# Optimization experiments

Measured on AMD Instinct MI355X. Metric: run time of the kernel, lower is better.

The kernel has to match this reference:

```python
import jax, jax.numpy as jnp
import numpy as np
from jax import lax

EPS = 0.1
CHANNEL = 1


def _sobel_kernels(channel):
    # sobel: 3x3, each row [-0.5, 0, 0.5] -> varies along width (w)
    s = jnp.array([[-0.5, 0.0, 0.5],
                   [-0.5, 0.0, 0.5],
                   [-0.5, 0.0, 0.5]], dtype=jnp.float32)
    kx = jnp.broadcast_to(s, (3, 3, 3))          # [d,h,w], constant over d,h; torch sobel.repeat(c,1,3,1,1)
    ky = jnp.broadcast_to(s.T, (3, 3, 3))        # varies along h
    kz = jnp.stack([jnp.full((3, 3), -0.5, jnp.float32),
                    jnp.zeros((3, 3), jnp.float32),
                    jnp.full((3, 3), 0.5, jnp.float32)], axis=0)  # varies along d
    def rep(k):
        return jnp.tile(k[None, None], (channel, 1, 1, 1, 1))  # [C,1,3,3,3] OIDHW
    return rep(kx), rep(ky), rep(kz)


def _grad3(x_pad, kernel, channel):
    # x_pad: [N,C,D+2,H+2,W+2]; cross-correlation matching F.conv3d, padding=0
    return lax.conv_general_dilated(
        x_pad, kernel, window_strides=(1, 1, 1), padding='VALID',
        dimension_numbers=('NCDHW', 'OIDHW', 'NCDHW'),
        feature_group_count=channel)


def setup_inputs() -> dict:
    key = jax.random.key(0)
    k1, k2 = jax.random.split(key)
    shape = (1, 1, 192, 224, 192)
    I = jax.random.normal(k1, shape, dtype=jnp.float32)
    J = jax.random.normal(k2, shape, dtype=jnp.float32)
    return {"I": I, "J": J}


def reference(I, J):
    kx, ky, kz = _sobel_kernels(CHANNEL)
    pad = ((0, 0), (0, 0), (1, 1), (1, 1), (1, 1))
    I_pad = jnp.pad(I, pad, mode='edge')  # ReplicationPad3d(1)
    J_pad = jnp.pad(J, pad, mode='edge')
    Ix = _grad3(I_pad, kx, CHANNEL)
    Iy = _grad3(I_pad, ky, CHANNEL)
    Iz = _grad3(I_pad, kz, CHANNEL)
    Jx = _grad3(J_pad, kx, CHANNEL)
    Jy = _grad3(J_pad, ky, CHANNEL)
    Jz = _grad3(J_pad, kz, CHANNEL)
    I_mag = Ix * Ix + Iy * Iy + Iz * Iz + EPS * EPS
    J_mag = Jx * Jx + Jy * Jy + Jz * Jz + EPS * EPS
    dot = Ix * Jx + Iy * Jy + Iz * Jz  # == sum over concat channel dim (C=1)
    ngf = (dot * dot) / (I_mag * J_mag)
    return jnp.mean(1.0 - ngf)
```

## Files before the change

### kernel.cpp

```cpp
#include <hip/hip_runtime.h>
#include <stdint.h>

#define DD 192
#define HH 224
#define WW 192
#define PLANE (HH*WW)
#define TOTAL (DD*HH*WW)

#define DSEG 6
#define NSEG (DD/DSEG)
#define NT 64
#define HPAIRS (HH/2)
#define NBLOCKS (HPAIRS*NSEG)

#define TILEF (4*WW)
#define BUFF (2*TILEF)
#define NPIECE 384
#define GUARD 4

typedef __attribute__((address_space(3))) uint32_t lds_t;
typedef __attribute__((address_space(1))) const uint32_t glb_t;

#define WAITV6()  asm volatile("s_waitcnt vmcnt(6)" ::: "memory")
#define WAITV0()  asm volatile("s_waitcnt vmcnt(0)" ::: "memory")
#define LGKM0()   asm volatile("s_waitcnt lgkmcnt(0)" ::: "memory")

struct PP {
    float IPT[6], IPS[6], IHD[6];
    float JPT[6], JPS[6], JHD[6];
};

__global__ __launch_bounds__(NT) void ngf_main_kernel(
    const float* __restrict__ I, const float* __restrict__ J,
    float* __restrict__ partial)
{
    __shared__ __align__(16) float lds[GUARD + 2 * BUFF + 4];
    const float EPS2 = 0.04f;

    int lane = threadIdx.x;

    int bid0 = blockIdx.x;
    int bid  = (bid0 & 7) * (NBLOCKS / 8) + (bid0 >> 3);

    int hb   = 2 * (bid % HPAIRS);
    int seg  = bid / HPAIRS;
    int ds   = seg * DSEG;

    const float* sp[6];
    int lo[6];
    #pragma unroll
    for (int m = 0; m < 6; ++m) {
        int p = lane + m * NT;
        int inp = (p >= NPIECE / 2) ? 1 : 0;
        int q   = p - inp * (NPIECE / 2);
        int r   = q / 48, c = q % 48;
        int srow = min(max(hb - 1 + r, 0), HH - 1);
        sp[m] = (inp ? J : I) + srow * WW + c * 4;
        lo[m] = GUARD + 4 * p;
    }

    auto stage = [&](int dp, int buf) {
        size_t poff = (size_t)dp * PLANE;
        #pragma unroll
        for (int m = 0; m < 6; ++m) {
            __builtin_amdgcn_global_load_lds((glb_t*)(sp[m] + poff),
                (lds_t*)(&lds[buf * BUFF + lo[m]]), 16, 0, 0);
        }
    };

    int l3 = 3 * lane;
    bool b0  = (lane == 0);
    bool b63 = (lane == 63);

    auto combine = [&](int buf) -> PP {
        PP P;
        #pragma unroll
        for (int j = 0; j < 6; ++j) {
            P.IPT[j] = 0.f; P.IPS[j] = 0.f; P.IHD[j] = 0.f;
            P.JPT[j] = 0.f; P.JPS[j] = 0.f; P.JHD[j] = 0.f;
        }
        const float* base = &lds[GUARD + buf * BUFF];
        #pragma unroll
        for (int b = 0; b < 4; ++b) {
            const float* BI = base + b * WW;
            const float* BJ = BI + TILEF;
            {
                float Lr = BI[l3 - 1];
                float x0 = BI[l3], x1 = BI[l3 + 1], x2 = BI[l3 + 2];
                float Rr = BI[l3 + 3];
                float L = b0  ? x0 : Lr;
                float R = b63 ? x2 : Rr;
                float s0 = L  + x0 + x1;
                float s1 = x0 + x1 + x2;
                float s2 = x1 + x2 + R;
                float t0 = x1 - L;
                float t1 = x2 - x0;
                float t2 = R  - x1;
                if (b <= 2) {
                    P.IPT[0] += t0; P.IPT[1] += t1; P.IPT[2] += t2;
                    P.IPS[0] += s0; P.IPS[1] += s1; P.IPS[2] += s2;
                    if (b == 0) { P.IHD[0] -= s0; P.IHD[1] -= s1; P.IHD[2] -= s2; }
                    if (b == 2) { P.IHD[0] += s0; P.IHD[1] += s1; P.IHD[2] += s2; }
                }
                if (b >= 1) {
                    P.IPT[3] += t0; P.IPT[4] += t1; P.IPT[5] += t2;
                    P.IPS[3] += s0; P.IPS[4] += s1; P.IPS[5] += s2;
                    if (b == 1) { P.IHD[3] -= s0; P.IHD[4] -= s1; P.IHD[5] -= s2; }
                    if (b == 3) { P.IHD[3] += s0; P.IHD[4] += s1; P.IHD[5] += s2; }
                }
            }
            {
                float Lr = BJ[l3 - 1];
                float x0 = BJ[l3], x1 = BJ[l3 + 1], x2 = BJ[l3 + 2];
                float Rr = BJ[l3 + 3];
                float L = b0  ? x0 : Lr;
                float R = b63 ? x2 : Rr;
                float s0 = L  + x0 + x1;
                float s1 = x0 + x1 + x2;
                float s2 = x1 + x2 + R;
                float t0 = x1 - L;
                float t1 = x2 - x0;
                float t2 = R  - x1;
                if (b <= 2) {
                    P.JPT[0] += t0; P.JPT[1] += t1; P.JPT[2] += t2;
                    P.JPS[0] += s0; P.JPS[1] += s1; P.JPS[2] += s2;
                    if (b == 0) { P.JHD[0] -= s0; P.JHD[1] -= s1; P.JHD[2] -= s2; }
                    if (b == 2) { P.JHD[0] += s0; P.JHD[1] += s1; P.JHD[2] += s2; }
                }
                if (b >= 1) {
                    P.JPT[3] += t0; P.JPT[4] += t1; P.JPT[5] += t2;
                    P.JPS[3] += s0; P.JPS[4] += s1; P.JPS[5] += s2;
                    if (b == 1) { P.JHD[3] -= s0; P.JHD[4] -= s1; P.JHD[5] -= s2; }
                    if (b == 3) { P.JHD[3] += s0; P.JHD[4] += s1; P.JHD[5] += s2; }
                }
            }
        }
        return P;
    };

    auto dcl = [&](int m) { return min(max(ds + m, 0), DD - 1); };

    float acc = 0.0f;
    PP p[3];

    auto ngf = [&](int k) {
        int sa = k % 3, sb2 = (k + 1) % 3, sc = (k + 2) % 3;
        #pragma unroll
        for (int j = 0; j < 6; ++j) {
            float Ix = p[sa].IPT[j] + p[sb2].IPT[j] + p[sc].IPT[j];
            float Iy = p[sa].IHD[j] + p[sb2].IHD[j] + p[sc].IHD[j];
            float Iz = p[sc].IPS[j] - p[sa].IPS[j];
            float Jx = p[sa].JPT[j] + p[sb2].JPT[j] + p[sc].JPT[j];
            float Jy = p[sa].JHD[j] + p[sb2].JHD[j] + p[sc].JHD[j];
            float Jz = p[sc].JPS[j] - p[sa].JPS[j];
            float Imag = fmaf(Ix, Ix, fmaf(Iy, Iy, fmaf(Iz, Iz, EPS2)));
            float Jmag = fmaf(Jx, Jx, fmaf(Jy, Jy, fmaf(Jz, Jz, EPS2)));
            float dot  = fmaf(Ix, Jx, fmaf(Iy, Jy, Iz * Jz));
            acc += 1.0f - (dot * dot) * __builtin_amdgcn_rcpf(Imag * Jmag);
        }
    };

    stage(dcl(-1), 0);
    stage(dcl(0), 1);
    WAITV6();
    p[0] = combine(0);
    LGKM0();
    stage(dcl(1), 0);
    WAITV6();
    p[1] = combine(1);
    LGKM0();
    stage(dcl(2), 1);

    #pragma unroll
    for (int k = 0; k < DSEG; ++k) {
        int buf = k & 1;
        if (k < DSEG - 1) { WAITV6(); }
        else             { WAITV0(); }
        __builtin_amdgcn_s_setprio(1);
        p[(k + 2) % 3] = combine(buf);
        __builtin_amdgcn_s_setprio(0);
        if (k <= DSEG - 3) {
            LGKM0();
            stage(dcl(k + 3), buf);
        }
        __builtin_amdgcn_s_setprio(1);
        ngf(k);
        __builtin_amdgcn_s_setprio(0);
    }

    #pragma unroll
    for (int o = 32; o > 0; o >>= 1)
        acc += __shfl_down(acc, o, 64);
    if (lane == 0)
        partial[bid] = acc;
}

__global__ __launch_bounds__(256) void ngf_reduce_kernel(
    const float* __restrict__ partial, float* __restrict__ out)
{
    double acc = 0.0;
    for (int i = threadIdx.x; i < NBLOCKS; i += blockDim.x)
        acc += (double)partial[i];

    #pragma unroll
    for (int o = 32; o > 0; o >>= 1)
        acc += __shfl_down(acc, o, 64);

    __shared__ double smem[4];
    int lane = threadIdx.x & 63;
    int wid  = threadIdx.x >> 6;
    if (lane == 0) smem[wid] = acc;
    __syncthreads();
    if (threadIdx.x == 0) {
        double s = smem[0] + smem[1] + smem[2] + smem[3];
        out[0] = (float)(s / (double)TOTAL);
    }
}

extern "C" void kernel_launch(void* const* d_in, const int* in_sizes, int n_in,
                              void* d_out, int out_size, void* d_ws, size_t ws_size,
                              hipStream_t stream)
{
    const float* I = (const float*)d_in[0];
    const float* J = (const float*)d_in[1];
    float* out = (float*)d_out;
    float* partial = (float*)d_ws;

    ngf_main_kernel<<<NBLOCKS, NT, 0, stream>>>(I, J, partial);
    ngf_reduce_kernel<<<1, 256, 0, stream>>>(partial, out);
}
```

Measured before the change: 29.18 us.

## Replace LDS double-buffered async staging with direct global loads

Removes the global_load_lds staging of four-row tiles into double-buffered shared memory, along with the manual waitcnt and setprio scheduling. Each lane now reads its three voxels plus neighbours straight from global memory through the cache, with edge clamping folded into precomputed offsets. This drops the LDS round trip and the explicit sync. The cost is that prefetch overlap is left to the compiler and hardware, and the loads become strided scalar loads per lane rather than 16-byte vector transfers.

Result: slower. 49.57 us (+69.8%).

```diff
diff --git a/kernel.cpp b/kernel.cpp
--- a/kernel.cpp
+++ b/kernel.cpp
@@ -13,17 +13,6 @@
 #define HPAIRS (HH/2)
 #define NBLOCKS (HPAIRS*NSEG)
 
-#define TILEF (4*WW)
-#define BUFF (2*TILEF)
-#define NPIECE 384
-#define GUARD 4
-
-typedef __attribute__((address_space(3))) uint32_t lds_t;
-typedef __attribute__((address_space(1))) const uint32_t glb_t;
-
-#define WAITV6()  asm volatile("s_waitcnt vmcnt(6)" ::: "memory")
-#define WAITV0()  asm volatile("s_waitcnt vmcnt(0)" ::: "memory")
-#define LGKM0()   asm volatile("s_waitcnt lgkmcnt(0)" ::: "memory")
 
 struct PP {
     float IPT[6], IPS[6], IHD[6];
@@ -34,7 +23,6 @@
     const float* __restrict__ I, const float* __restrict__ J,
     float* __restrict__ partial)
 {
-    __shared__ __align__(16) float lds[GUARD + 2 * BUFF + 4];
     const float EPS2 = 0.04f;
 
     int lane = threadIdx.x;
@@ -46,50 +34,31 @@
     int seg  = bid / HPAIRS;
     int ds   = seg * DSEG;
 
-    const float* sp[6];
-    int lo[6];
+    int srow[4];
     #pragma unroll
-    for (int m = 0; m < 6; ++m) {
-        int p = lane + m * NT;
-        int inp = (p >= NPIECE / 2) ? 1 : 0;
-        int q   = p - inp * (NPIECE / 2);
-        int r   = q / 48, c = q % 48;
-        int srow = min(max(hb - 1 + r, 0), HH - 1);
-        sp[m] = (inp ? J : I) + srow * WW + c * 4;
-        lo[m] = GUARD + 4 * p;
-    }
+    for (int r = 0; r < 4; ++r)
+        srow[r] = min(max(hb - 1 + r, 0), HH - 1);
 
-    auto stage = [&](int dp, int buf) {
-        size_t poff = (size_t)dp * PLANE;
-        #pragma unroll
-        for (int m = 0; m < 6; ++m) {
-            __builtin_amdgcn_global_load_lds((glb_t*)(sp[m] + poff),
-                (lds_t*)(&lds[buf * BUFF + lo[m]]), 16, 0, 0);
-        }
-    };
+    int l3   = 3 * lane;
+    int offL = l3 + ((lane == 0)  ? 0 : -1);
+    int offR = l3 + ((lane == 63) ? 2 :  3);
 
-    int l3 = 3 * lane;
-    bool b0  = (lane == 0);
-    bool b63 = (lane == 63);
-
-    auto combine = [&](int buf) -> PP {
+    auto combine = [&](int dp) -> PP {
         PP P;
         #pragma unroll
         for (int j = 0; j < 6; ++j) {
             P.IPT[j] = 0.f; P.IPS[j] = 0.f; P.IHD[j] = 0.f;
             P.JPT[j] = 0.f; P.JPS[j] = 0.f; P.JHD[j] = 0.f;
         }
-        const float* base = &lds[GUARD + buf * BUFF];
+        size_t poff = (size_t)dp * PLANE;
         #pragma unroll
         for (int b = 0; b < 4; ++b) {
-            const float* BI = base + b * WW;
-            const float* BJ = BI + TILEF;
+            const float* RI = I + poff + srow[b] * WW;
+            const float* RJ = J + poff + srow[b] * WW;
             {
-                float Lr = BI[l3 - 1];
-                float x0 = BI[l3], x1 = BI[l3 + 1], x2 = BI[l3 + 2];
-                float Rr = BI[l3 + 3];
-                float L = b0  ? x0 : Lr;
-                float R = b63 ? x2 : Rr;
+                float L  = RI[offL];
+                float x0 = RI[l3], x1 = RI[l3 + 1], x2 = RI[l3 + 2];
+                float R  = RI[offR];
                 float s0 = L  + x0 + x1;
                 float s1 = x0 + x1 + x2;
                 float s2 = x1 + x2 + R;
@@ -110,11 +79,9 @@
                 }
             }
             {
-                float Lr = BJ[l3 - 1];
-                float x0 = BJ[l3], x1 = BJ[l3 + 1], x2 = BJ[l3 + 2];
-                float Rr = BJ[l3 + 3];
-                float L = b0  ? x0 : Lr;
-                float R = b63 ? x2 : Rr;
+                float L  = RJ[offL];
+                float x0 = RJ[l3], x1 = RJ[l3 + 1], x2 = RJ[l3 + 2];
+                float R  = RJ[offR];
                 float s0 = L  + x0 + x1;
                 float s1 = x0 + x1 + x2;
                 float s2 = x1 + x2 + R;
@@ -160,32 +127,12 @@
         }
     };
 
-    stage(dcl(-1), 0);
-    stage(dcl(0), 1);
-    WAITV6();
-    p[0] = combine(0);
-    LGKM0();
-    stage(dcl(1), 0);
-    WAITV6();
-    p[1] = combine(1);
-    LGKM0();
-    stage(dcl(2), 1);
-
+    p[0] = combine(dcl(-1));
+    p[1] = combine(dcl(0));
     #pragma unroll
     for (int k = 0; k < DSEG; ++k) {
-        int buf = k & 1;
-        if (k < DSEG - 1) { WAITV6(); }
-        else             { WAITV0(); }
-        __builtin_amdgcn_s_setprio(1);
-        p[(k + 2) % 3] = combine(buf);
-        __builtin_amdgcn_s_setprio(0);
-        if (k <= DSEG - 3) {
-            LGKM0();
-            stage(dcl(k + 3), buf);
-        }
-        __builtin_amdgcn_s_setprio(1);
+        p[(k + 2) % 3] = combine(dcl(k + 1));
         ngf(k);
-        __builtin_amdgcn_s_setprio(0);
     }
 
     #pragma unroll
```
